# Kernel optimization log

Measured on AMD Instinct MI355X. Metric: run time of the kernel, lower is better.

## Reference

```python
import jax, jax.numpy as jnp
import numpy as np

N_NODES = 100000
N_EDGES = 3200000
EMB = 64
K = 2
NUM_GRAPHS = 512


def setup_inputs() -> dict:
    key = jax.random.key(0)
    ks = jax.random.split(key, 12)
    x = jax.random.normal(ks[0], (N_NODES, EMB), dtype=jnp.float32)
    edge_index = jax.random.randint(ks[1], (2, N_EDGES), 0, N_NODES, dtype=jnp.int64)
    edge_attr = jax.random.normal(ks[2], (N_EDGES, 1), dtype=jnp.float32)
    batch = jnp.sort(jax.random.randint(ks[3], (N_NODES,), 0, NUM_GRAPHS, dtype=jnp.int64))
    s = 1.0 / np.sqrt(EMB)
    wn1 = jax.random.normal(ks[4], (EMB, EMB), dtype=jnp.float32) * s
    bn1 = jnp.zeros((EMB,), jnp.float32)
    wn2 = jax.random.normal(ks[5], (EMB, 1), dtype=jnp.float32) * s
    bn2 = jnp.zeros((1,), jnp.float32)
    wc1 = jax.random.normal(ks[6], (EMB, EMB), dtype=jnp.float32) * s
    bc1 = jnp.zeros((EMB,), jnp.float32)
    wc2 = jax.random.normal(ks[7], (EMB, 2 * K * EMB), dtype=jnp.float32) * s
    bc2 = jnp.zeros((2 * K * EMB,), jnp.float32)
    return dict(x=x, edge_index=edge_index, edge_attr=edge_attr, batch=batch,
                wn1=wn1, bn1=bn1, wn2=wn2, bn2=bn2,
                wc1=wc1, bc1=bc1, wc2=wc2, bc2=bc2)


def reference(x, edge_index, edge_attr, batch, wn1, bn1, wn2, bn2, wc1, bc1, wc2, bc2):
    N, C = x.shape
    alpha = 0.1  # APPNP teleport prob
    # --- APPNP(K=1): gcn_norm with self-loops, one propagation step ---
    loops = jnp.arange(N, dtype=edge_index.dtype)
    src = jnp.concatenate([edge_index[0], loops])
    dst = jnp.concatenate([edge_index[1], loops])
    ones = jnp.ones(src.shape[0], dtype=x.dtype)
    deg = jax.ops.segment_sum(ones, dst, num_segments=N)
    dinv = jnp.where(deg > 0, jax.lax.rsqrt(deg), 0.0)
    norm = dinv[src] * dinv[dst]  # [E+N]
    agg = jax.ops.segment_sum(x[src] * norm[:, None], dst, num_segments=N)
    diffuse_x = (1.0 - alpha) * agg + alpha * x  # [N, C]
    # --- node-wise gate: MLP -> global softmax over all nodes ---
    h = jax.nn.relu(diffuse_x @ wn1 + bn1)
    gamma = h @ wn2 + bn2  # [N, 1]
    gamma = jax.nn.softmax(gamma, axis=0)
    # --- per-graph mean pool + channel-wise MLP ---
    sums = jax.ops.segment_sum(diffuse_x, batch, num_segments=NUM_GRAPHS)
    cnt = jax.ops.segment_sum(jnp.ones((N,), x.dtype), batch, num_segments=NUM_GRAPHS)
    pooled = jnp.where(cnt[:, None] > 0, sums / jnp.maximum(cnt, 1.0)[:, None], 0.0)
    pc = jnp.tanh(jax.nn.relu(pooled @ wc1 + bc1) @ wc2 + bc2)  # [B, 2*K*C]
    alpha_kc = pc[:, : K * C].reshape(NUM_GRAPHS, K, C)
    beta_kc = alpha_kc  # faithful to original bug: beta_kc = alpha_kc.reshape(...)
    # --- per-node affine via kron(alpha_kc, gamma_dense) gathered back to nodes ---
    # alpha_batch[b, n, k, c] = alpha_kc[b, k, c] * gamma_dense[b, n]; mask-gather == index by batch
    g = gamma[:, :, None]  # [N, 1, 1]
    a_node = alpha_kc[batch] * g  # [N, K, C]
    b_node = beta_kc[batch] * g  # [N, K, C]
    out = jnp.max(a_node * x[:, None, :] + b_node, axis=1)  # [N, C]
    return out
```

## Files before the change

kernel.cpp:

```cpp
#include <hip/hip_runtime.h>
#include <cstdint>

#define N_NODES   100000
#define N_EDGES   3200000
#define EMB       64
#define NUM_GRAPHS 512
#define NB        391
#define CAP       9216
#define PCHUNK    4096
#define PBLOCKS   ((N_EDGES + PCHUNK - 1) / PCHUNK)
#define CVTBLKS   ((N_NODES * EMB / 2 + 255) / 256)

__device__ __forceinline__ float bflo(unsigned u) { return __uint_as_float(u << 16); }
__device__ __forceinline__ float bfhi(unsigned u) { return __uint_as_float(u & 0xFFFF0000u); }
__device__ __forceinline__ unsigned rne_bf16(float f) {
    unsigned b = __float_as_uint(f);
    return (b + 0x7FFFu + ((b >> 16) & 1u)) >> 16;
}

__global__ void build_kernel(const int* __restrict__ ei, int* __restrict__ bcnt,
                             unsigned* __restrict__ gpairs,
                             const float* __restrict__ x, unsigned* __restrict__ xh) {
    __shared__ unsigned sp[PCHUNK];
    __shared__ unsigned short sb[PCHUNK];
    __shared__ int scnt[512];
    __shared__ int soff[512];
    __shared__ int scur[512];
    __shared__ int gbase[512];
    __shared__ int s[256];
    int t = threadIdx.x;

    if (blockIdx.x >= PBLOCKS) {
        int i = (blockIdx.x - PBLOCKS) * 256 + t;
        if (i < N_NODES * EMB / 2) {
            float2 f = ((const float2*)x)[i];
            xh[i] = rne_bf16(f.x) | (rne_bf16(f.y) << 16);
        }
        return;
    }

    for (int i = t; i < 512; i += 256) scnt[i] = 0;
    __syncthreads();
    int base = blockIdx.x * PCHUNK;
    int lim  = min(N_EDGES - base, PCHUNK);
    for (int k = t; k < lim; k += 256) {
        int d = ei[N_EDGES + base + k];
        atomicAdd(&scnt[d >> 8], 1);
    }
    __syncthreads();
    int a0 = scnt[2 * t], a1 = scnt[2 * t + 1];
    int p = a0 + a1;
    s[t] = p; __syncthreads();
    for (int d = 1; d < 256; d <<= 1) {
        int add = (t >= d) ? s[t - d] : 0;
        __syncthreads();
        s[t] += add;
        __syncthreads();
    }
    int excl = s[t] - p;
    soff[2 * t] = excl;       soff[2 * t + 1] = excl + a0;
    scur[2 * t] = excl;       scur[2 * t + 1] = excl + a0;
    __syncthreads();
    for (int i = t; i < NB; i += 256) gbase[i] = i * CAP + atomicAdd(&bcnt[i], scnt[i]);
    __syncthreads();
    for (int k = t; k < lim; k += 256) {
        int sId = ei[base + k];
        int d   = ei[N_EDGES + base + k];
        int b   = d >> 8;
        int pos = atomicAdd(&scur[b], 1);
        sp[pos] = (unsigned)sId | ((unsigned)(d & 255) << 17);
        sb[pos] = (unsigned short)b;
    }
    __syncthreads();
    for (int i = t; i < lim; i += 256) {
        int b = sb[i];
        gpairs[gbase[b] + (i - soff[b])] = sp[i];
    }
}

__global__ void build_kernel_f32(const int* __restrict__ ei, int* __restrict__ bcnt,
                                 unsigned* __restrict__ gpairs) {
    __shared__ unsigned sp[PCHUNK];
    __shared__ unsigned short sb[PCHUNK];
    __shared__ int scnt[512];
    __shared__ int soff[512];
    __shared__ int scur[512];
    __shared__ int gbase[512];
    __shared__ int s[256];
    int t = threadIdx.x;
    for (int i = t; i < 512; i += 256) scnt[i] = 0;
    __syncthreads();
    int base = blockIdx.x * PCHUNK;
    int lim  = min(N_EDGES - base, PCHUNK);
    for (int k = t; k < lim; k += 256) {
        int d = ei[N_EDGES + base + k];
        atomicAdd(&scnt[d >> 8], 1);
    }
    __syncthreads();
    int a0 = scnt[2 * t], a1 = scnt[2 * t + 1];
    int p = a0 + a1;
    s[t] = p; __syncthreads();
    for (int d = 1; d < 256; d <<= 1) {
        int add = (t >= d) ? s[t - d] : 0;
        __syncthreads();
        s[t] += add;
        __syncthreads();
    }
    int excl = s[t] - p;
    soff[2 * t] = excl;       soff[2 * t + 1] = excl + a0;
    scur[2 * t] = excl;       scur[2 * t + 1] = excl + a0;
    __syncthreads();
    for (int i = t; i < NB; i += 256) gbase[i] = i * CAP + atomicAdd(&bcnt[i], scnt[i]);
    __syncthreads();
    for (int k = t; k < lim; k += 256) {
        int sId = ei[base + k];
        int d   = ei[N_EDGES + base + k];
        int b   = d >> 8;
        int pos = atomicAdd(&scur[b], 1);
        sp[pos] = (unsigned)sId | ((unsigned)(d & 255) << 17);
        sb[pos] = (unsigned short)b;
    }
    __syncthreads();
    for (int i = t; i < lim; i += 256) {
        int b = sb[i];
        gpairs[gbase[b] + (i - soff[b])] = sp[i];
    }
}

__global__ void bscatter2_kernel(const unsigned* __restrict__ gpairs, const int* __restrict__ bcnt,
                                 int* __restrict__ ebuf,
                                 int* __restrict__ indeg, int* __restrict__ rowstart,
                                 float* __restrict__ dinv) {
    int b = blockIdx.x, t = threadIdx.x, nlo = b << 8;
    __shared__ int pref[512];
    __shared__ int lcnt[256];
    __shared__ int lcur[256];
    __shared__ int s[256];

    int c0 = (2 * t < NB) ? bcnt[2 * t] : 0;
    int c1 = (2 * t + 1 < NB) ? bcnt[2 * t + 1] : 0;
    int pp = c0 + c1;
    s[t] = pp; __syncthreads();
    for (int d = 1; d < 256; d <<= 1) {
        int add = (t >= d) ? s[t - d] : 0;
        __syncthreads();
        s[t] += add;
        __syncthreads();
    }
    int excl2 = s[t] - pp;
    pref[2 * t] = excl2;
    pref[2 * t + 1] = excl2 + c0;
    lcnt[t] = 0;
    __syncthreads();
    int base = pref[b];

    int cnt = bcnt[b];
    const unsigned* gp = gpairs + (size_t)b * CAP;
    for (int i = t; i < cnt; i += 256) atomicAdd(&lcnt[(gp[i] >> 17) & 255], 1);
    __syncthreads();
    int v = lcnt[t];
    s[t] = v; __syncthreads();
    for (int d = 1; d < 256; d <<= 1) {
        int add = (t >= d) ? s[t - d] : 0;
        __syncthreads();
        s[t] += add;
        __syncthreads();
    }
    int excl = s[t] - v;
    int n = nlo + t;
    if (n < N_NODES) {
        indeg[n] = v;
        rowstart[n] = base + excl;
        dinv[n] = rsqrtf((float)(v + 1));
    }
    lcur[t] = base + excl;
    __syncthreads();
    for (int i = t; i < cnt; i += 256) {
        unsigned pk = gp[i];
        int pos = atomicAdd(&lcur[(pk >> 17) & 255], 1);
        ebuf[pos] = (int)(pk & 0x1FFFFu);
    }
}

__global__ void gather_mlp_bf16(const int* __restrict__ ebuf, const int* __restrict__ rowstart,
                                const int* __restrict__ indeg, const float* __restrict__ dinv,
                                const float* __restrict__ x, const unsigned* __restrict__ xh,
                                float* __restrict__ dx,
                                const float* __restrict__ wn1, const float* __restrict__ bn1,
                                const float* __restrict__ wn2, const float* __restrict__ bn2,
                                float* __restrict__ gl) {
    __shared__ float wn1s[EMB * EMB];
    __shared__ float bn1s[EMB];
    __shared__ float wn2s[EMB];
    for (int i = threadIdx.x; i < EMB * EMB; i += blockDim.x) wn1s[i] = wn1[i];
    if (threadIdx.x < EMB) { bn1s[threadIdx.x] = bn1[threadIdx.x]; wn2s[threadIdx.x] = wn2[threadIdx.x]; }
    __syncthreads();

    int wid = (blockIdx.x * blockDim.x + threadIdx.x) >> 6;
    if (wid >= N_NODES) return;
    int n = __builtin_amdgcn_readfirstlane(wid);
    int l = threadIdx.x & 63;
    int g = l >> 3;
    int q = l & 7;
    int start = rowstart[n];
    int cnt   = indeg[n];
    float dn  = dinv[n];
    const uint4* __restrict__ xr = (const uint4*)xh;

    float a0 = 0.f, a1 = 0.f, a2 = 0.f, a3 = 0.f, a4 = 0.f, a5 = 0.f, a6 = 0.f, a7 = 0.f;
    int j = 0;
    for (; j + 32 <= cnt; j += 32) {
        int sA = ebuf[start + j + g];
        int sB = ebuf[start + j + 8 + g];
        int sC = ebuf[start + j + 16 + g];
        int sD = ebuf[start + j + 24 + g];
        float wA = dinv[sA] * dn;
        float wB = dinv[sB] * dn;
        float wC = dinv[sC] * dn;
        float wD = dinv[sD] * dn;
        uint4 vA = xr[sA * 8 + q];
        uint4 vB = xr[sB * 8 + q];
        uint4 vC = xr[sC * 8 + q];
        uint4 vD = xr[sD * 8 + q];
        a0 += bflo(vA.x) * wA + bflo(vB.x) * wB + bflo(vC.x) * wC + bflo(vD.x) * wD;
        a1 += bfhi(vA.x) * wA + bfhi(vB.x) * wB + bfhi(vC.x) * wC + bfhi(vD.x) * wD;
        a2 += bflo(vA.y) * wA + bflo(vB.y) * wB + bflo(vC.y) * wC + bflo(vD.y) * wD;
        a3 += bfhi(vA.y) * wA + bfhi(vB.y) * wB + bfhi(vC.y) * wC + bfhi(vD.y) * wD;
        a4 += bflo(vA.z) * wA + bflo(vB.z) * wB + bflo(vC.z) * wC + bflo(vD.z) * wD;
        a5 += bfhi(vA.z) * wA + bfhi(vB.z) * wB + bfhi(vC.z) * wC + bfhi(vD.z) * wD;
        a6 += bflo(vA.w) * wA + bflo(vB.w) * wB + bflo(vC.w) * wC + bflo(vD.w) * wD;
        a7 += bfhi(vA.w) * wA + bfhi(vB.w) * wB + bfhi(vC.w) * wC + bfhi(vD.w) * wD;
    }
    if (j + 16 <= cnt) {
        int sA = ebuf[start + j + g];
        int sB = ebuf[start + j + 8 + g];
        float wA = dinv[sA] * dn;
        float wB = dinv[sB] * dn;
        uint4 vA = xr[sA * 8 + q];
        uint4 vB = xr[sB * 8 + q];
        a0 += bflo(vA.x) * wA + bflo(vB.x) * wB;
        a1 += bfhi(vA.x) * wA + bfhi(vB.x) * wB;
        a2 += bflo(vA.y) * wA + bflo(vB.y) * wB;
        a3 += bfhi(vA.y) * wA + bfhi(vB.y) * wB;
        a4 += bflo(vA.z) * wA + bflo(vB.z) * wB;
        a5 += bfhi(vA.z) * wA + bfhi(vB.z) * wB;
        a6 += bflo(vA.w) * wA + bflo(vB.w) * wB;
        a7 += bfhi(vA.w) * wA + bfhi(vB.w) * wB;
        j += 16;
    }
    if (j + 8 <= cnt) {
        int sA = ebuf[start + j + g];
        float wA = dinv[sA] * dn;
        uint4 vA = xr[sA * 8 + q];
        a0 += bflo(vA.x) * wA; a1 += bfhi(vA.x) * wA;
        a2 += bflo(vA.y) * wA; a3 += bfhi(vA.y) * wA;
        a4 += bflo(vA.z) * wA; a5 += bfhi(vA.z) * wA;
        a6 += bflo(vA.w) * wA; a7 += bfhi(vA.w) * wA;
        j += 8;
    }
    if (g < cnt - j) {
        int sA = ebuf[start + j + g];
        float wA = dinv[sA] * dn;
        uint4 vA = xr[sA * 8 + q];
        a0 += bflo(vA.x) * wA; a1 += bfhi(vA.x) * wA;
        a2 += bflo(vA.y) * wA; a3 += bfhi(vA.y) * wA;
        a4 += bflo(vA.z) * wA; a5 += bfhi(vA.z) * wA;
        a6 += bflo(vA.w) * wA; a7 += bfhi(vA.w) * wA;
    }
    a0 += __shfl_xor(a0, 8); a0 += __shfl_xor(a0, 16); a0 += __shfl_xor(a0, 32);
    a1 += __shfl_xor(a1, 8); a1 += __shfl_xor(a1, 16); a1 += __shfl_xor(a1, 32);
    a2 += __shfl_xor(a2, 8); a2 += __shfl_xor(a2, 16); a2 += __shfl_xor(a2, 32);
    a3 += __shfl_xor(a3, 8); a3 += __shfl_xor(a3, 16); a3 += __shfl_xor(a3, 32);
    a4 += __shfl_xor(a4, 8); a4 += __shfl_xor(a4, 16); a4 += __shfl_xor(a4, 32);
    a5 += __shfl_xor(a5, 8); a5 += __shfl_xor(a5, 16); a5 += __shfl_xor(a5, 32);
    a6 += __shfl_xor(a6, 8); a6 += __shfl_xor(a6, 16); a6 += __shfl_xor(a6, 32);
    a7 += __shfl_xor(a7, 8); a7 += __shfl_xor(a7, 16); a7 += __shfl_xor(a7, 32);

    const float4* __restrict__ x4 = (const float4*)x;
    float4 xv0 = x4[n * 16 + 2 * q];
    float4 xv1 = x4[n * 16 + 2 * q + 1];
    float s2 = dn * dn;
    float r0 = 0.9f * (a0 + xv0.x * s2) + 0.1f * xv0.x;
    float r1 = 0.9f * (a1 + xv0.y * s2) + 0.1f * xv0.y;
    float r2 = 0.9f * (a2 + xv0.z * s2) + 0.1f * xv0.z;
    float r3 = 0.9f * (a3 + xv0.w * s2) + 0.1f * xv0.w;
    float r4 = 0.9f * (a4 + xv1.x * s2) + 0.1f * xv1.x;
    float r5 = 0.9f * (a5 + xv1.y * s2) + 0.1f * xv1.y;
    float r6 = 0.9f * (a6 + xv1.z * s2) + 0.1f * xv1.z;
    float r7 = 0.9f * (a7 + xv1.w * s2) + 0.1f * xv1.w;
    if (l < 8) {
        float4 w0; w0.x = r0; w0.y = r1; w0.z = r2; w0.w = r3;
        float4 w1; w1.x = r4; w1.y = r5; w1.z = r6; w1.w = r7;
        ((float4*)dx)[n * 16 + 2 * l]     = w0;
        ((float4*)dx)[n * 16 + 2 * l + 1] = w1;
    }

    float rr[8] = {r0, r1, r2, r3, r4, r5, r6, r7};
    float am = bn1s[l];
#pragma unroll
    for (int c = 0; c < EMB; ++c) {
        float b = __shfl(rr[c & 7], c >> 3);
        am += b * wn1s[c * EMB + l];
    }
    float h = fmaxf(am, 0.0f);
    float t = h * wn2s[l];
#pragma unroll
    for (int off = 32; off; off >>= 1) t += __shfl_xor(t, off);
    if (l == 0) gl[n] = t + bn2[0];
}

__global__ void gather_mlp_kernel(const int* __restrict__ ebuf, const int* __restrict__ rowstart,
                                  const int* __restrict__ indeg, const float* __restrict__ dinv,
                                  const float* __restrict__ x, float* __restrict__ dx,
                                  const float* __restrict__ wn1, const float* __restrict__ bn1,
                                  const float* __restrict__ wn2, const float* __restrict__ bn2,
                                  float* __restrict__ gl) {
    __shared__ float wn1s[EMB * EMB];
    __shared__ float bn1s[EMB];
    __shared__ float wn2s[EMB];
    for (int i = threadIdx.x; i < EMB * EMB; i += blockDim.x) wn1s[i] = wn1[i];
    if (threadIdx.x < EMB) { bn1s[threadIdx.x] = bn1[threadIdx.x]; wn2s[threadIdx.x] = wn2[threadIdx.x]; }
    __syncthreads();

    int wid = (blockIdx.x * blockDim.x + threadIdx.x) >> 6;
    if (wid >= N_NODES) return;
    int n = __builtin_amdgcn_readfirstlane(wid);
    int l = threadIdx.x & 63;
    int g = l >> 4;
    int q = l & 15;
    int start = rowstart[n];
    int cnt   = indeg[n];
    float dn  = dinv[n];
    const float4* __restrict__ x4 = (const float4*)x;

    float ax = 0.f, ay = 0.f, az = 0.f, aw = 0.f;
    int j = 0;
    for (; j + 8 <= cnt; j += 8) {
        int sA = ebuf[start + j + g];
        int sB = ebuf[start + j + 4 + g];
        float wA = dinv[sA] * dn;
        float wB = dinv[sB] * dn;
        float4 vA = x4[sA * 16 + q];
        float4 vB = x4[sB * 16 + q];
        ax += vA.x * wA + vB.x * wB;
        ay += vA.y * wA + vB.y * wB;
        az += vA.z * wA + vB.z * wB;
        aw += vA.w * wA + vB.w * wB;
    }
    if (j + 4 <= cnt) {
        int sA = ebuf[start + j + g];
        float wA = dinv[sA] * dn;
        float4 vA = x4[sA * 16 + q];
        ax += vA.x * wA; ay += vA.y * wA; az += vA.z * wA; aw += vA.w * wA;
        j += 4;
    }
    int rem = cnt - j;
    if (g < rem) {
        int sA = ebuf[start + j + g];
        float wA = dinv[sA] * dn;
        float4 vA = x4[sA * 16 + q];
        ax += vA.x * wA; ay += vA.y * wA; az += vA.z * wA; aw += vA.w * wA;
    }
    ax += __shfl_xor(ax, 16); ax += __shfl_xor(ax, 32);
    ay += __shfl_xor(ay, 16); ay += __shfl_xor(ay, 32);
    az += __shfl_xor(az, 16); az += __shfl_xor(az, 32);
    aw += __shfl_xor(aw, 16); aw += __shfl_xor(aw, 32);

    float4 xv = x4[n * 16 + q];
    float s2 = dn * dn;
    float r0 = 0.9f * (ax + xv.x * s2) + 0.1f * xv.x;
    float r1 = 0.9f * (ay + xv.y * s2) + 0.1f * xv.y;
    float r2 = 0.9f * (az + xv.z * s2) + 0.1f * xv.z;
    float r3 = 0.9f * (aw + xv.w * s2) + 0.1f * xv.w;
    if (l < 16) {
        float4 rv; rv.x = r0; rv.y = r1; rv.z = r2; rv.w = r3;
        ((float4*)dx)[n * 16 + q] = rv;
    }
    float rr[4] = {r0, r1, r2, r3};
    float am = bn1s[l];
#pragma unroll
    for (int c = 0; c < EMB; ++c) {
        float b = __shfl(rr[c & 3], c >> 2);
        am += b * wn1s[c * EMB + l];
    }
    float h = fmaxf(am, 0.0f);
    float t = h * wn2s[l];
#pragma unroll
    for (int off = 32; off; off >>= 1) t += __shfl_xor(t, off);
    if (l == 0) gl[n] = t + bn2[0];
}

__device__ inline int lower_bound_i(const int* a, int n, int key) {
    int lo = 0, hi = n;
    while (lo < hi) {
        int mid = (lo + hi) >> 1;
        if (a[mid] < key) lo = mid + 1; else hi = mid;
    }
    return lo;
}
__global__ void poolexp_kernel(const float* __restrict__ dx, const int* __restrict__ batch,
                               const float* __restrict__ wc1, const float* __restrict__ bc1,
                               const float* __restrict__ wc2, const float* __restrict__ bc2,
                               float* __restrict__ alphag,
                               const float* __restrict__ gl, float* __restrict__ gsum) {
    __shared__ float red[4][EMB];
    __shared__ float p[EMB];
    __shared__ float h[EMB];
    __shared__ float red1[256];

    if (blockIdx.x >= NUM_GRAPHS) {
        int vb = blockIdx.x - NUM_GRAPHS;
        float s = 0.0f;
        for (int i = vb * 256 + threadIdx.x; i < N_NODES; i += 256 * 256)
            s += expf(gl[i]);
        red1[threadIdx.x] = s; __syncthreads();
        for (int t = 128; t; t >>= 1) {
            if ((int)threadIdx.x < t) red1[threadIdx.x] += red1[threadIdx.x + t];
            __syncthreads();
        }
        if (threadIdx.x == 0) atomicAdd(gsum, red1[0]);
        return;
    }

    int g = blockIdx.x;
    int lo = lower_bound_i(batch, N_NODES, g);
    int hi = lower_bound_i(batch, N_NODES, g + 1);
    int lane = threadIdx.x & 63;
    int w = threadIdx.x >> 6;
    float acc = 0.0f;
    for (int n = lo + w; n < hi; n += 4) acc += dx[n * EMB + lane];
    red[w][lane] = acc; __syncthreads();
    if (threadIdx.x < EMB) {
        float s = red[0][threadIdx.x] + red[1][threadIdx.x] + red[2][threadIdx.x] + red[3][threadIdx.x];
        int cnt = hi - lo;
        p[threadIdx.x] = cnt > 0 ? s / (float)cnt : 0.0f;
    }
    __syncthreads();
    if (threadIdx.x < EMB) {
        int j = threadIdx.x;
        float a = bc1[j];
        for (int c = 0; c < EMB; ++c) a += p[c] * wc1[c * EMB + j];
        h[j] = fmaxf(a, 0.0f);
    }
    __syncthreads();
    if (threadIdx.x < 128) {
        int o = threadIdx.x;
        float a = bc2[o];
        for (int j = 0; j < EMB; ++j) a += h[j] * wc2[j * 256 + o];
        alphag[g * 128 + o] = tanhf(a);
    }
}

__global__ void final_kernel(const float* __restrict__ x, const int* __restrict__ batch,
                             const float* __restrict__ gl, const float* __restrict__ gsum,
                             const float* __restrict__ alphag, float* __restrict__ out) {
    int n = (blockIdx.x * blockDim.x + threadIdx.x) >> 6;
    if (n >= N_NODES) return;
    int lane = threadIdx.x & 63;
    int g = batch[n];
    float gamma = expf(gl[n]) / gsum[0];
    float a0 = alphag[g * 128 + lane];
    float a1 = alphag[g * 128 + 64 + lane];
    float t = gamma * (x[n * EMB + lane] + 1.0f);
    out[n * EMB + lane] = fmaxf(a0 * t, a1 * t);
}

extern "C" void kernel_launch(void* const* d_in, const int* in_sizes, int n_in,
                              void* d_out, int out_size, void* d_ws, size_t ws_size,
                              hipStream_t stream) {
    const float* x     = (const float*)d_in[0];
    const int*   ei    = (const int*)d_in[1];
    const int*   batch = (const int*)d_in[3];
    const float* wn1 = (const float*)d_in[4];
    const float* bn1 = (const float*)d_in[5];
    const float* wn2 = (const float*)d_in[6];
    const float* bn2 = (const float*)d_in[7];
    const float* wc1 = (const float*)d_in[8];
    const float* bc1 = (const float*)d_in[9];
    const float* wc2 = (const float*)d_in[10];
    const float* bc2 = (const float*)d_in[11];
    float* out = (float*)d_out;

    char* wsb = (char*)d_ws;
    float* dx     = (float*)wsb;
    float* gl     = dx + (size_t)N_NODES * EMB;
    float* dinv   = gl + N_NODES;
    float* pooled = dinv + N_NODES;
    float* alphag = pooled + NUM_GRAPHS * EMB;
    int*   bcnt   = (int*)(alphag + NUM_GRAPHS * 128);
    float* gsum   = (float*)(bcnt + 512);
    int*   bbase  = (int*)(gsum + 1);
    int*   indeg  = bbase + 512;
    int*   rowstart = indeg + N_NODES;
    int*   ebuf   = rowstart + N_NODES;
    unsigned* xh  = (unsigned*)(ebuf + N_EDGES);
    unsigned* gpairs = (unsigned*)dx;

    size_t need_bf16 = (size_t)((char*)(xh + (size_t)N_NODES * EMB / 2) - wsb);
    int use_bf16 = (ws_size >= need_bf16);

    hipMemsetAsync(bcnt, 0, 513 * sizeof(int), stream);
    if (use_bf16)
        build_kernel<<<PBLOCKS + CVTBLKS, 256, 0, stream>>>(ei, bcnt, gpairs, x, xh);
    else
        build_kernel_f32<<<PBLOCKS, 256, 0, stream>>>(ei, bcnt, gpairs);
    bscatter2_kernel<<<NB, 256, 0, stream>>>(gpairs, bcnt, ebuf, indeg, rowstart, dinv);
    if (use_bf16)
        gather_mlp_bf16<<<(N_NODES * 64) / 256, 256, 0, stream>>>(ebuf, rowstart, indeg, dinv, x, xh, dx,
                                                                  wn1, bn1, wn2, bn2, gl);
    else
        gather_mlp_kernel<<<(N_NODES * 64) / 256, 256, 0, stream>>>(ebuf, rowstart, indeg, dinv, x, dx,
                                                                    wn1, bn1, wn2, bn2, gl);
    poolexp_kernel<<<NUM_GRAPHS + 256, 256, 0, stream>>>(dx, batch, wc1, bc1, wc2, bc2, alphag, gl, gsum);
    final_kernel<<<N_NODES / 4, 256, 0, stream>>>(x, batch, gl, gsum, alphag, out);
}
```

Before: 286.2 us.

## Slice bf16 features into four channel planes and split gather from node MLP

The bf16 copy of x is stored as four separate 16-channel slices, each node taking 32 bytes per slice. The gather runs one block per slice and lets 32 edges share a wave, so each slice's working set is a quarter of the feature table and should fit better in cache. The node MLP moves into its own kernel that re-reads dx. This costs an extra launch, a second full read of dx, and reading each node's edge list four times.

```diff
diff --git a/kernel.cpp b/kernel.cpp
--- a/kernel.cpp
+++ b/kernel.cpp
@@ -9,7 +9,7 @@
 #define CAP       9216
 #define PCHUNK    4096
 #define PBLOCKS   ((N_EDGES + PCHUNK - 1) / PCHUNK)
-#define CVTBLKS   ((N_NODES * EMB / 2 + 255) / 256)
+#define CVTBLKS   ((N_NODES * 32 + 255) / 256)
 
 __device__ __forceinline__ float bflo(unsigned u) { return __uint_as_float(u << 16); }
 __device__ __forceinline__ float bfhi(unsigned u) { return __uint_as_float(u & 0xFFFF0000u); }
@@ -20,7 +20,7 @@
 
 __global__ void build_kernel(const int* __restrict__ ei, int* __restrict__ bcnt,
                              unsigned* __restrict__ gpairs,
-                             const float* __restrict__ x, unsigned* __restrict__ xh) {
+                             const float* __restrict__ x, unsigned* __restrict__ xs) {
     __shared__ unsigned sp[PCHUNK];
     __shared__ unsigned short sb[PCHUNK];
     __shared__ int scnt[512];
@@ -32,9 +32,12 @@
 
     if (blockIdx.x >= PBLOCKS) {
         int i = (blockIdx.x - PBLOCKS) * 256 + t;
-        if (i < N_NODES * EMB / 2) {
+        if (i < N_NODES * 32) {
+            int n = i >> 5, k = i & 31;
             float2 f = ((const float2*)x)[i];
-            xh[i] = rne_bf16(f.x) | (rne_bf16(f.y) << 16);
+            unsigned u = rne_bf16(f.x) | (rne_bf16(f.y) << 16);
+            int slice = k >> 3, uu = k & 7;
+            xs[((size_t)slice * N_NODES + n) * 8 + uu] = u;
         }
         return;
     }
@@ -182,10 +185,72 @@
     }
 }
 
-__global__ void gather_mlp_bf16(const int* __restrict__ ebuf, const int* __restrict__ rowstart,
-                                const int* __restrict__ indeg, const float* __restrict__ dinv,
-                                const float* __restrict__ x, const unsigned* __restrict__ xh,
-                                float* __restrict__ dx,
+__global__ void gather4_bf16(const int* __restrict__ ebuf, const int* __restrict__ rowstart,
+                             const int* __restrict__ indeg, const float* __restrict__ dinv,
+                             const unsigned* __restrict__ xs, const float* __restrict__ x,
+                             float* __restrict__ dx) {
+    int slice = blockIdx.x & 3;
+    int node  = (blockIdx.x >> 2) * 4 + (threadIdx.x >> 6);
+    if (node >= N_NODES) return;
+    int l = threadIdx.x & 63;
+    int q = l & 1;
+    int e = l >> 1;
+    int start = rowstart[node];
+    int cnt   = indeg[node];
+    float dn  = dinv[node];
+    const uint4* __restrict__ xs4 = ((const uint4*)xs) + (size_t)slice * N_NODES * 2;
+
+    float a0 = 0.f, a1 = 0.f, a2 = 0.f, a3 = 0.f, a4 = 0.f, a5 = 0.f, a6 = 0.f, a7 = 0.f;
+    int j = 0;
+    for (; j + 32 <= cnt; j += 32) {
+        int sA = ebuf[start + j + e];
+        float wA = dinv[sA] * dn;
+        uint4 v = xs4[sA * 2 + q];
+        a0 += bflo(v.x) * wA; a1 += bfhi(v.x) * wA;
+        a2 += bflo(v.y) * wA; a3 += bfhi(v.y) * wA;
+        a4 += bflo(v.z) * wA; a5 += bfhi(v.z) * wA;
+        a6 += bflo(v.w) * wA; a7 += bfhi(v.w) * wA;
+    }
+    if (e < cnt - j) {
+        int sA = ebuf[start + j + e];
+        float wA = dinv[sA] * dn;
+        uint4 v = xs4[sA * 2 + q];
+        a0 += bflo(v.x) * wA; a1 += bfhi(v.x) * wA;
+        a2 += bflo(v.y) * wA; a3 += bfhi(v.y) * wA;
+        a4 += bflo(v.z) * wA; a5 += bfhi(v.z) * wA;
+        a6 += bflo(v.w) * wA; a7 += bfhi(v.w) * wA;
+    }
+    a0 += __shfl_xor(a0, 2); a1 += __shfl_xor(a1, 2); a2 += __shfl_xor(a2, 2); a3 += __shfl_xor(a3, 2);
+    a4 += __shfl_xor(a4, 2); a5 += __shfl_xor(a5, 2); a6 += __shfl_xor(a6, 2); a7 += __shfl_xor(a7, 2);
+    a0 += __shfl_xor(a0, 4); a1 += __shfl_xor(a1, 4); a2 += __shfl_xor(a2, 4); a3 += __shfl_xor(a3, 4);
+    a4 += __shfl_xor(a4, 4); a5 += __shfl_xor(a5, 4); a6 += __shfl_xor(a6, 4); a7 += __shfl_xor(a7, 4);
+    a0 += __shfl_xor(a0, 8); a1 += __shfl_xor(a1, 8); a2 += __shfl_xor(a2, 8); a3 += __shfl_xor(a3, 8);
+    a4 += __shfl_xor(a4, 8); a5 += __shfl_xor(a5, 8); a6 += __shfl_xor(a6, 8); a7 += __shfl_xor(a7, 8);
+    a0 += __shfl_xor(a0, 16); a1 += __shfl_xor(a1, 16); a2 += __shfl_xor(a2, 16); a3 += __shfl_xor(a3, 16);
+    a4 += __shfl_xor(a4, 16); a5 += __shfl_xor(a5, 16); a6 += __shfl_xor(a6, 16); a7 += __shfl_xor(a7, 16);
+    a0 += __shfl_xor(a0, 32); a1 += __shfl_xor(a1, 32); a2 += __shfl_xor(a2, 32); a3 += __shfl_xor(a3, 32);
+    a4 += __shfl_xor(a4, 32); a5 += __shfl_xor(a5, 32); a6 += __shfl_xor(a6, 32); a7 += __shfl_xor(a7, 32);
+
+    if (l < 2) {
+        const float4* __restrict__ x4f = (const float4*)x;
+        float4 xv0 = x4f[node * 16 + slice * 4 + l * 2];
+        float4 xv1 = x4f[node * 16 + slice * 4 + l * 2 + 1];
+        float s2 = dn * dn;
+        float4 w0, w1;
+        w0.x = 0.9f * (a0 + xv0.x * s2) + 0.1f * xv0.x;
+        w0.y = 0.9f * (a1 + xv0.y * s2) + 0.1f * xv0.y;
+        w0.z = 0.9f * (a2 + xv0.z * s2) + 0.1f * xv0.z;
+        w0.w = 0.9f * (a3 + xv0.w * s2) + 0.1f * xv0.w;
+        w1.x = 0.9f * (a4 + xv1.x * s2) + 0.1f * xv1.x;
+        w1.y = 0.9f * (a5 + xv1.y * s2) + 0.1f * xv1.y;
+        w1.z = 0.9f * (a6 + xv1.z * s2) + 0.1f * xv1.z;
+        w1.w = 0.9f * (a7 + xv1.w * s2) + 0.1f * xv1.w;
+        ((float4*)dx)[node * 16 + slice * 4 + l * 2]     = w0;
+        ((float4*)dx)[node * 16 + slice * 4 + l * 2 + 1] = w1;
+    }
+}
+
+__global__ void node_mlp_kernel(const float* __restrict__ dx,
                                 const float* __restrict__ wn1, const float* __restrict__ bn1,
                                 const float* __restrict__ wn2, const float* __restrict__ bn2,
                                 float* __restrict__ gl) {
@@ -195,118 +260,21 @@
     for (int i = threadIdx.x; i < EMB * EMB; i += blockDim.x) wn1s[i] = wn1[i];
     if (threadIdx.x < EMB) { bn1s[threadIdx.x] = bn1[threadIdx.x]; wn2s[threadIdx.x] = wn2[threadIdx.x]; }
     __syncthreads();
-
-    int wid = (blockIdx.x * blockDim.x + threadIdx.x) >> 6;
-    if (wid >= N_NODES) return;
-    int n = __builtin_amdgcn_readfirstlane(wid);
-    int l = threadIdx.x & 63;
-    int g = l >> 3;
-    int q = l & 7;
-    int start = rowstart[n];
-    int cnt   = indeg[n];
-    float dn  = dinv[n];
-    const uint4* __restrict__ xr = (const uint4*)xh;
-
-    float a0 = 0.f, a1 = 0.f, a2 = 0.f, a3 = 0.f, a4 = 0.f, a5 = 0.f, a6 = 0.f, a7 = 0.f;
-    int j = 0;
-    for (; j + 32 <= cnt; j += 32) {
-        int sA = ebuf[start + j + g];
-        int sB = ebuf[start + j + 8 + g];
-        int sC = ebuf[start + j + 16 + g];
-        int sD = ebuf[start + j + 24 + g];
-        float wA = dinv[sA] * dn;
-        float wB = dinv[sB] * dn;
-        float wC = dinv[sC] * dn;
-        float wD = dinv[sD] * dn;
-        uint4 vA = xr[sA * 8 + q];
-        uint4 vB = xr[sB * 8 + q];
-        uint4 vC = xr[sC * 8 + q];
-        uint4 vD = xr[sD * 8 + q];
-        a0 += bflo(vA.x) * wA + bflo(vB.x) * wB + bflo(vC.x) * wC + bflo(vD.x) * wD;
-        a1 += bfhi(vA.x) * wA + bfhi(vB.x) * wB + bfhi(vC.x) * wC + bfhi(vD.x) * wD;
-        a2 += bflo(vA.y) * wA + bflo(vB.y) * wB + bflo(vC.y) * wC + bflo(vD.y) * wD;
-        a3 += bfhi(vA.y) * wA + bfhi(vB.y) * wB + bfhi(vC.y) * wC + bfhi(vD.y) * wD;
-        a4 += bflo(vA.z) * wA + bflo(vB.z) * wB + bflo(vC.z) * wC + bflo(vD.z) * wD;
-        a5 += bfhi(vA.z) * wA + bfhi(vB.z) * wB + bfhi(vC.z) * wC + bfhi(vD.z) * wD;
-        a6 += bflo(vA.w) * wA + bflo(vB.w) * wB + bflo(vC.w) * wC + bflo(vD.w) * wD;
-        a7 += bfhi(vA.w) * wA + bfhi(vB.w) * wB + bfhi(vC.w) * wC + bfhi(vD.w) * wD;
-    }
-    if (j + 16 <= cnt) {
-        int sA = ebuf[start + j + g];
-        int sB = ebuf[start + j + 8 + g];
-        float wA = dinv[sA] * dn;
-        float wB = dinv[sB] * dn;
-        uint4 vA = xr[sA * 8 + q];
-        uint4 vB = xr[sB * 8 + q];
-        a0 += bflo(vA.x) * wA + bflo(vB.x) * wB;
-        a1 += bfhi(vA.x) * wA + bfhi(vB.x) * wB;
-        a2 += bflo(vA.y) * wA + bflo(vB.y) * wB;
-        a3 += bfhi(vA.y) * wA + bfhi(vB.y) * wB;
-        a4 += bflo(vA.z) * wA + bflo(vB.z) * wB;
-        a5 += bfhi(vA.z) * wA + bfhi(vB.z) * wB;
-        a6 += bflo(vA.w) * wA + bflo(vB.w) * wB;
-        a7 += bfhi(vA.w) * wA + bfhi(vB.w) * wB;
-        j += 16;
-    }
-    if (j + 8 <= cnt) {
-        int sA = ebuf[start + j + g];
-        float wA = dinv[sA] * dn;
-        uint4 vA = xr[sA * 8 + q];
-        a0 += bflo(vA.x) * wA; a1 += bfhi(vA.x) * wA;
-        a2 += bflo(vA.y) * wA; a3 += bfhi(vA.y) * wA;
-        a4 += bflo(vA.z) * wA; a5 += bfhi(vA.z) * wA;
-        a6 += bflo(vA.w) * wA; a7 += bfhi(vA.w) * wA;
-        j += 8;
-    }
-    if (g < cnt - j) {
-        int sA = ebuf[start + j + g];
-        float wA = dinv[sA] * dn;
-        uint4 vA = xr[sA * 8 + q];
-        a0 += bflo(vA.x) * wA; a1 += bfhi(vA.x) * wA;
-        a2 += bflo(vA.y) * wA; a3 += bfhi(vA.y) * wA;
-        a4 += bflo(vA.z) * wA; a5 += bfhi(vA.z) * wA;
-        a6 += bflo(vA.w) * wA; a7 += bfhi(vA.w) * wA;
-    }
-    a0 += __shfl_xor(a0, 8); a0 += __shfl_xor(a0, 16); a0 += __shfl_xor(a0, 32);
-    a1 += __shfl_xor(a1, 8); a1 += __shfl_xor(a1, 16); a1 += __shfl_xor(a1, 32);
-    a2 += __shfl_xor(a2, 8); a2 += __shfl_xor(a2, 16); a2 += __shfl_xor(a2, 32);
-    a3 += __shfl_xor(a3, 8); a3 += __shfl_xor(a3, 16); a3 += __shfl_xor(a3, 32);
-    a4 += __shfl_xor(a4, 8); a4 += __shfl_xor(a4, 16); a4 += __shfl_xor(a4, 32);
-    a5 += __shfl_xor(a5, 8); a5 += __shfl_xor(a5, 16); a5 += __shfl_xor(a5, 32);
-    a6 += __shfl_xor(a6, 8); a6 += __shfl_xor(a6, 16); a6 += __shfl_xor(a6, 32);
-    a7 += __shfl_xor(a7, 8); a7 += __shfl_xor(a7, 16); a7 += __shfl_xor(a7, 32);
-
-    const float4* __restrict__ x4 = (const float4*)x;
-    float4 xv0 = x4[n * 16 + 2 * q];
-    float4 xv1 = x4[n * 16 + 2 * q + 1];
-    float s2 = dn * dn;
-    float r0 = 0.9f * (a0 + xv0.x * s2) + 0.1f * xv0.x;
-    float r1 = 0.9f * (a1 + xv0.y * s2) + 0.1f * xv0.y;
-    float r2 = 0.9f * (a2 + xv0.z * s2) + 0.1f * xv0.z;
-    float r3 = 0.9f * (a3 + xv0.w * s2) + 0.1f * xv0.w;
-    float r4 = 0.9f * (a4 + xv1.x * s2) + 0.1f * xv1.x;
-    float r5 = 0.9f * (a5 + xv1.y * s2) + 0.1f * xv1.y;
-    float r6 = 0.9f * (a6 + xv1.z * s2) + 0.1f * xv1.z;
-    float r7 = 0.9f * (a7 + xv1.w * s2) + 0.1f * xv1.w;
-    if (l < 8) {
-        float4 w0; w0.x = r0; w0.y = r1; w0.z = r2; w0.w = r3;
-        float4 w1; w1.x = r4; w1.y = r5; w1.z = r6; w1.w = r7;
-        ((float4*)dx)[n * 16 + 2 * l]     = w0;
-        ((float4*)dx)[n * 16 + 2 * l + 1] = w1;
-    }
-
-    float rr[8] = {r0, r1, r2, r3, r4, r5, r6, r7};
-    float am = bn1s[l];
+    int n = (blockIdx.x * blockDim.x + threadIdx.x) >> 6;
+    if (n >= N_NODES) return;
+    int j = threadIdx.x & 63;
+    float rowv = dx[n * EMB + j];
+    float acc = bn1s[j];
 #pragma unroll
     for (int c = 0; c < EMB; ++c) {
-        float b = __shfl(rr[c & 7], c >> 3);
-        am += b * wn1s[c * EMB + l];
-    }
-    float h = fmaxf(am, 0.0f);
-    float t = h * wn2s[l];
+        float b = __shfl(rowv, c);
+        acc += b * wn1s[c * EMB + j];
+    }
+    float h = fmaxf(acc, 0.0f);
+    float t = h * wn2s[j];
 #pragma unroll
     for (int off = 32; off; off >>= 1) t += __shfl_xor(t, off);
-    if (l == 0) gl[n] = t + bn2[0];
+    if (j == 0) gl[n] = t + bn2[0];
 }
 
 __global__ void gather_mlp_kernel(const int* __restrict__ ebuf, const int* __restrict__ rowstart,
@@ -493,24 +461,25 @@
     int*   indeg  = bbase + 512;
     int*   rowstart = indeg + N_NODES;
     int*   ebuf   = rowstart + N_NODES;
-    unsigned* xh  = (unsigned*)(ebuf + N_EDGES);
+    unsigned* xs  = (unsigned*)(ebuf + N_EDGES);
     unsigned* gpairs = (unsigned*)dx;
 
-    size_t need_bf16 = (size_t)((char*)(xh + (size_t)N_NODES * EMB / 2) - wsb);
+    size_t need_bf16 = (size_t)((char*)(xs + (size_t)N_NODES * EMB / 2) - wsb);
     int use_bf16 = (ws_size >= need_bf16);
 
     hipMemsetAsync(bcnt, 0, 513 * sizeof(int), stream);
     if (use_bf16)
-        build_kernel<<<PBLOCKS + CVTBLKS, 256, 0, stream>>>(ei, bcnt, gpairs, x, xh);
+        build_kernel<<<PBLOCKS + CVTBLKS, 256, 0, stream>>>(ei, bcnt, gpairs, x, xs);
     else
         build_kernel_f32<<<PBLOCKS, 256, 0, stream>>>(ei, bcnt, gpairs);
     bscatter2_kernel<<<NB, 256, 0, stream>>>(gpairs, bcnt, ebuf, indeg, rowstart, dinv);
-    if (use_bf16)
-        gather_mlp_bf16<<<(N_NODES * 64) / 256, 256, 0, stream>>>(ebuf, rowstart, indeg, dinv, x, xh, dx,
-                                                                  wn1, bn1, wn2, bn2, gl);
-    else
+    if (use_bf16) {
+        gather4_bf16<<<((N_NODES + 3) / 4) * 4, 256, 0, stream>>>(ebuf, rowstart, indeg, dinv, xs, x, dx);
+        node_mlp_kernel<<<(N_NODES * 64) / 256, 256, 0, stream>>>(dx, wn1, bn1, wn2, bn2, gl);
+    } else {
         gather_mlp_kernel<<<(N_NODES * 64) / 256, 256, 0, stream>>>(ebuf, rowstart, indeg, dinv, x, dx,
                                                                     wn1, bn1, wn2, bn2, gl);
+    }
     poolexp_kernel<<<NUM_GRAPHS + 256, 256, 0, stream>>>(dx, batch, wc1, bc1, wc2, bc2, alphag, gl, gsum);
     final_kernel<<<N_NODES / 4, 256, 0, stream>>>(x, batch, gl, gsum, alphag, out);
 }
```

After: 408.9 us. +42.9%, slower.
